# Performance work log

Measured on AMD Instinct MI355X. Metric: run time of the kernel, lower is better.

Reference implementation:

```python
import jax, jax.numpy as jnp
import numpy as np

B, S, D = 2, 2048, 2048
H, KVH = 16, 8
HD = D // H          # 128
REP = H // KVH       # 2
FF = 5504
EPS = 1e-5
THETA = 1e6


def rotate_half(x):
    h = x.shape[-1] // 2
    return jnp.concatenate([-x[..., h:], x[..., :h]], axis=-1)


def rms_norm(x, g):
    v = jnp.mean(x.astype(jnp.float32) ** 2, axis=-1, keepdims=True)
    return (x * jax.lax.rsqrt(v + EPS)).astype(x.dtype) * g


def setup_inputs() -> dict:
    key = jax.random.key(0)
    ks = jax.random.split(key, 10)
    # RoPE tables [S, HD]
    inv_freq = 1.0 / (THETA ** (np.arange(0, HD, 2, dtype=np.float32) / HD))
    t = np.arange(S, dtype=np.float32)
    freqs = np.outer(t, inv_freq)                      # [S, HD/2]
    emb = np.concatenate([freqs, freqs], axis=-1)      # [S, HD]
    sc = 0.02
    return {
        "x": jax.random.normal(ks[0], (B, S, D), jnp.float32),
        "cos": jnp.asarray(np.cos(emb)),
        "sin": jnp.asarray(np.sin(emb)),
        "wq": jax.random.normal(ks[1], (H * HD, D), jnp.float32) * sc,
        "wk": jax.random.normal(ks[2], (KVH * HD, D), jnp.float32) * sc,
        "wv": jax.random.normal(ks[3], (KVH * HD, D), jnp.float32) * sc,
        "wo": jax.random.normal(ks[4], (D, H * HD), jnp.float32) * sc,
        "w_gate": jax.random.normal(ks[5], (FF, D), jnp.float32) * sc,
        "w_up": jax.random.normal(ks[6], (FF, D), jnp.float32) * sc,
        "w_down": jax.random.normal(ks[7], (D, FF), jnp.float32) * sc,
        "g1": jnp.ones((D,), jnp.float32),
        "g2": jnp.ones((D,), jnp.float32),
    }


def reference(x, cos, sin, wq, wk, wv, wo, w_gate, w_up, w_down, g1, g2):
    # ---- attention sub-block ----
    h = rms_norm(x, g1)
    q = (h @ wq.T).reshape(B, S, H, HD)
    k = (h @ wk.T).reshape(B, S, KVH, HD)
    v = (h @ wv.T).reshape(B, S, KVH, HD)
    # RoPE: cos/sin [S,HD] -> broadcast over (B, S, heads, HD) via unsqueeze at head dim
    c = cos[:S][:, None, :]
    s = sin[:S][:, None, :]
    q = q * c + rotate_half(q) * s
    k = k * c + rotate_half(k) * s
    # GQA repeat_kv (repeat_interleave on head dim), then bshd -> bhsd
    k = jnp.repeat(k, REP, axis=2).transpose(0, 2, 1, 3)
    v = jnp.repeat(v, REP, axis=2).transpose(0, 2, 1, 3)
    q = q.transpose(0, 2, 1, 3)
    scores = jnp.einsum("bhqd,bhkd->bhqk", q, k) / jnp.sqrt(jnp.float32(HD))
    causal = jnp.triu(jnp.full((S, S), -jnp.inf, jnp.float32), k=1)
    scores = scores + causal[None, None]
    attn = jax.nn.softmax(scores.astype(jnp.float32), axis=-1).astype(scores.dtype)
    out = jnp.einsum("bhqk,bhkd->bhqd", attn, v)
    out = out.transpose(0, 2, 1, 3).reshape(B, S, H * HD)
    x = x + out @ wo.T
    # ---- SwiGLU MLP sub-block ----
    h2 = rms_norm(x, g2)
    mlp = (jax.nn.silu(h2 @ w_gate.T) * (h2 @ w_up.T)) @ w_down.T
    return x + mlp
```

## Files before the change

### kernel.cpp

```cpp
#include <hip/hip_runtime.h>


#define DM 2048
#define SEQ 2048
#define HD 128
#define FF_ 5504
#define QK_SCALE_L2E 0.12751744f

typedef __bf16 bf16x8 __attribute__((ext_vector_type(8)));
typedef float f32x4 __attribute__((ext_vector_type(4)));
typedef float f32x16 __attribute__((ext_vector_type(16)));
typedef unsigned short u16x8 __attribute__((ext_vector_type(8)));
typedef unsigned int u32x4 __attribute__((ext_vector_type(4)));

typedef __attribute__((address_space(1))) void* gas1;
typedef __attribute__((address_space(3))) void* las3;
#define GLDS16(g, s) __builtin_amdgcn_global_load_lds((gas1)(g), (las3)(s), 16, 0, 0)

static __device__ __forceinline__ float bf2f(unsigned short u) {
  union { unsigned int i; float f; } c; c.i = ((unsigned int)u) << 16; return c.f;
}
static __device__ __forceinline__ unsigned short f2bf(float f) {
  __bf16 b = (__bf16)f;
  return __builtin_bit_cast(unsigned short, b);
}
static __device__ __forceinline__ unsigned int pk2(float a, float b) {
  return (unsigned int)f2bf(a) | ((unsigned int)f2bf(b) << 16);
}
static __device__ __forceinline__ float fexp2(float x) { return exp2f(x); }

__global__ __launch_bounds__(256) void k_conv(const float* __restrict__ src,
                                              unsigned short* __restrict__ dst) {
  size_t i = (size_t)(blockIdx.x * 256 + threadIdx.x) * 8;
  float4 a = *(const float4*)&src[i];
  float4 b = *(const float4*)&src[i + 4];
  u16x8 o;
  o[0] = f2bf(a.x); o[1] = f2bf(a.y); o[2] = f2bf(a.z); o[3] = f2bf(a.w);
  o[4] = f2bf(b.x); o[5] = f2bf(b.y); o[6] = f2bf(b.z); o[7] = f2bf(b.w);
  *(u16x8*)&dst[i] = o;
}

__global__ __launch_bounds__(256) void k_conv_gu(const float* __restrict__ g,
                                                 const float* __restrict__ u,
                                                 unsigned short* __restrict__ dst) {
  int i = blockIdx.x * 256 + threadIdx.x;
  int row = i >> 8;
  int c8 = (i & 255) * 8;
  int t = row >> 8, r = row & 255;
  const float* src = (r < 128) ? (g + (size_t)(t * 128 + r) * DM + c8)
                               : (u + (size_t)(t * 128 + (r - 128)) * DM + c8);
  float4 a = *(const float4*)src;
  float4 b = *(const float4*)(src + 4);
  u16x8 o;
  o[0] = f2bf(a.x); o[1] = f2bf(a.y); o[2] = f2bf(a.z); o[3] = f2bf(a.w);
  o[4] = f2bf(b.x); o[5] = f2bf(b.y); o[6] = f2bf(b.z); o[7] = f2bf(b.w);
  *(u16x8*)&dst[(size_t)row * DM + c8] = o;
}

__global__ __launch_bounds__(256) void k_rmsnorm(const float* __restrict__ x,
                                                 const float* __restrict__ g,
                                                 unsigned short* __restrict__ out) {
  int row = blockIdx.x, tid = threadIdx.x;
  const float* xr = x + (size_t)row * DM;
  float4 a = *(const float4*)&xr[tid * 8];
  float4 b = *(const float4*)&xr[tid * 8 + 4];
  float ss = a.x * a.x + a.y * a.y + a.z * a.z + a.w * a.w +
             b.x * b.x + b.y * b.y + b.z * b.z + b.w * b.w;
#pragma unroll
  for (int off = 32; off > 0; off >>= 1) ss += __shfl_xor(ss, off, 64);
  __shared__ float red[4];
  if ((tid & 63) == 0) red[tid >> 6] = ss;
  __syncthreads();
  float rs = rsqrtf((red[0] + red[1] + red[2] + red[3]) * (1.0f / DM) + 1e-5f);
  float4 ga = *(const float4*)&g[tid * 8];
  float4 gb = *(const float4*)&g[tid * 8 + 4];
  u16x8 o;
  o[0] = f2bf(a.x * rs * ga.x); o[1] = f2bf(a.y * rs * ga.y);
  o[2] = f2bf(a.z * rs * ga.z); o[3] = f2bf(a.w * rs * ga.w);
  o[4] = f2bf(b.x * rs * gb.x); o[5] = f2bf(b.y * rs * gb.y);
  o[6] = f2bf(b.z * rs * gb.z); o[7] = f2bf(b.w * rs * gb.w);
  *(u16x8*)&out[(size_t)row * DM + tid * 8] = o;
}

__global__ __launch_bounds__(256) void k_rope(unsigned short* __restrict__ qkv,
                                              const float* __restrict__ cosT,
                                              const float* __restrict__ sinT) {
  int idx = blockIdx.x * 256 + threadIdx.x;
  int j = idx & 63;
  int hh = (idx >> 6) % 24;
  int tok = idx / (64 * 24);
  int s = tok & (SEQ - 1);
  int colbase = (hh < 16) ? hh * HD : DM + (hh - 16) * HD;
  unsigned short* p = qkv + (size_t)tok * 4096 + colbase;
  float lo = bf2f(p[j]), hi = bf2f(p[j + 64]);
  const float* cr = cosT + (size_t)s * HD;
  const float* sr = sinT + (size_t)s * HD;
  float nl = lo * cr[j] - hi * sr[j];
  float nh = hi * cr[j + 64] + lo * sr[j + 64];
  if (hh < 16) { nl *= QK_SCALE_L2E; nh *= QK_SCALE_L2E; }
  p[j] = f2bf(nl);
  p[j + 64] = f2bf(nh);
}

template <int BN, int EPI, int PIPE>
__global__ __launch_bounds__(512, 2) void k_gemm8(
    const unsigned short* __restrict__ A, const unsigned short* __restrict__ Bt,
    unsigned short* __restrict__ outB, float* __restrict__ outF,
    const float* __restrict__ res, int N, int K) {
  constexpr int NF = BN / 64;
  constexpr int BSTMT = BN / 128;
  constexpr int ABY = 256 * 64;
  constexpr int BBY = BN * 64;
  constexpr int BUF = ABY + BBY;
  constexpr int VPK = 2 + BSTMT;
  constexpr int NBUF = PIPE ? 2 : 4;
  __shared__ __attribute__((aligned(16))) unsigned char smem[NBUF * BUF];

  const int tid = threadIdx.x, w = tid >> 6, l = tid & 63;
  const int wr = w >> 2, wc = w & 3, lr = l & 15, lg = l >> 4;
  const int nwg = gridDim.x, bid = blockIdx.x;
  const int bswz = (bid & 7) * (nwg >> 3) + (bid >> 3);
  const int mt = bswz & 15, nt = bswz >> 4;
  const int m0 = mt * 256, n0 = nt * BN;
  const int nk = K >> 5;

  const int srow = w * 16 + (l >> 2);
  const int sg8 = ((l & 3) ^ ((l >> 3) & 3)) * 8;
  const unsigned short* Asrc = A + (size_t)(m0 + srow) * K + sg8;
  const unsigned short* Bsrc = Bt + (size_t)(n0 + srow) * K + sg8;
  const int aoff = (wr * 128 + lr) * 64 + ((lg ^ ((lr >> 1) & 3)) << 4);
  const int boff = (wc * (BN / 4) + lr) * 64 + ((lg ^ ((lr >> 1) & 3)) << 4);

  auto stageA = [&](int kt) {
    unsigned char* bb = smem + (kt & (NBUF - 1)) * BUF;
#pragma unroll
    for (int i = 0; i < 2; i++)
      GLDS16(Asrc + (size_t)i * 128 * K + kt * 32, bb + (i * 512 + w * 64) * 16);
  };
  auto stageB = [&](int kt) {
    unsigned char* bb = smem + (kt & (NBUF - 1)) * BUF + ABY;
#pragma unroll
    for (int i = 0; i < BSTMT; i++)
      GLDS16(Bsrc + (size_t)i * 128 * K + kt * 32, bb + (i * 512 + w * 64) * 16);
  };

  f32x4 acc[8][NF] = {};

  if constexpr (PIPE == 1) {
    stageA(0); stageB(0);
    asm volatile("s_waitcnt vmcnt(0)" ::: "memory");
    __builtin_amdgcn_s_barrier();
    for (int kt = 0; kt < nk; kt++) {
      unsigned char* ba = smem + (kt & 1) * BUF;
      unsigned char* bb = ba + ABY;
      if (kt + 1 < nk) { stageA(kt + 1); stageB(kt + 1); }
      bf16x8 am[8], bnf[NF];
#pragma unroll
      for (int m = 0; m < 8; m++) am[m] = *(const bf16x8*)(ba + aoff + m * 1024);
#pragma unroll
      for (int n = 0; n < NF; n++) bnf[n] = *(const bf16x8*)(bb + boff + n * 1024);
      __builtin_amdgcn_s_setprio(1);
#pragma unroll
      for (int m = 0; m < 8; m++)
#pragma unroll
        for (int n = 0; n < NF; n++)
          acc[m][n] = __builtin_amdgcn_mfma_f32_16x16x32_bf16(am[m], bnf[n], acc[m][n], 0, 0, 0);
      __builtin_amdgcn_s_setprio(0);
      asm volatile("s_waitcnt vmcnt(0)" ::: "memory");
      __builtin_amdgcn_s_barrier();
    }
  } else {
    for (int kt = 0; kt < 3; kt++) { stageA(kt); stageB(kt); }
    asm volatile("s_waitcnt vmcnt(%0)" ::"i"(2 * VPK) : "memory");
    __builtin_amdgcn_s_barrier();
    for (int kt = 0; kt < nk; kt++) {
      unsigned char* ba = smem + (kt & 3) * BUF;
      unsigned char* bb = ba + ABY;
      const bool st = (kt + 3) < nk;
      bf16x8 am[8], bnf[NF];
#pragma unroll
      for (int m = 0; m < 8; m++) am[m] = *(const bf16x8*)(ba + aoff + m * 1024);
#pragma unroll
      for (int n = 0; n < NF; n++) bnf[n] = *(const bf16x8*)(bb + boff + n * 1024);
      if (st) { stageA(kt + 3); stageB(kt + 3); }
      __builtin_amdgcn_s_barrier();
      __builtin_amdgcn_s_setprio(1);
#pragma unroll
      for (int m = 0; m < 8; m++)
#pragma unroll
        for (int n = 0; n < NF; n++)
          acc[m][n] = __builtin_amdgcn_mfma_f32_16x16x32_bf16(am[m], bnf[n], acc[m][n], 0, 0, 0);
      __builtin_amdgcn_s_setprio(0);
      if (kt <= nk - 4)      asm volatile("s_waitcnt vmcnt(%0)" ::"i"(2 * VPK) : "memory");
      else if (kt == nk - 3) asm volatile("s_waitcnt vmcnt(%0)" ::"i"(VPK) : "memory");
      else if (kt == nk - 2) asm volatile("s_waitcnt vmcnt(0)" ::: "memory");
      __builtin_amdgcn_s_barrier();
    }
  }

  const int rbase = wr * 128 + lg * 4;
  const int cbase = wc * (BN / 4) + lr;
  if constexpr (EPI == 0) {
#pragma unroll
    for (int m = 0; m < 8; m++)
#pragma unroll
      for (int n = 0; n < NF; n++)
#pragma unroll
        for (int j = 0; j < 4; j++)
          outB[(size_t)(m0 + rbase + m * 16 + j) * N + n0 + cbase + n * 16] =
              f2bf(acc[m][n][j]);
  } else if constexpr (EPI == 1) {
#pragma unroll
    for (int m = 0; m < 8; m++)
#pragma unroll
      for (int n = 0; n < NF; n++)
#pragma unroll
        for (int j = 0; j < 4; j++) {
          size_t o = (size_t)(m0 + rbase + m * 16 + j) * N + n0 + cbase + n * 16;
          outF[o] = res[o] + acc[m][n][j];
        }
  } else {
    float* gl = (float*)smem;
    const int ab = n0 >> 1;
    __syncthreads();
#pragma unroll
    for (int half = 0; half < 2; half++) {
      if (wr == half && wc < 2) {
#pragma unroll
        for (int m = 0; m < 8; m++)
#pragma unroll
          for (int n = 0; n < NF; n++)
#pragma unroll
            for (int j = 0; j < 4; j++)
              gl[(m * 16 + lg * 4 + j) * 128 + wc * 64 + n * 16 + lr] = acc[m][n][j];
      }
      __syncthreads();
      if (wr == half && wc >= 2) {
#pragma unroll
        for (int m = 0; m < 8; m++)
#pragma unroll
          for (int n = 0; n < NF; n++)
#pragma unroll
            for (int j = 0; j < 4; j++) {
              int rl = m * 16 + lg * 4 + j;
              int cl = (wc - 2) * 64 + n * 16 + lr;
              float g = gl[rl * 128 + cl];
              float s = g / (1.0f + __expf(-g));
              outB[(size_t)(m0 + half * 128 + rl) * FF_ + ab + cl] = f2bf(s * acc[m][n][j]);
            }
      }
      __syncthreads();
    }
  }
}

__global__ __launch_bounds__(256) void k_attn2(const unsigned short* __restrict__ qkv,
                                               unsigned short* __restrict__ out) {
  __shared__ __attribute__((aligned(16))) unsigned short lK[2][64 * 128];
  __shared__ __attribute__((aligned(16))) unsigned short lV[2][128 * 64];
  const float NEG = -3.0e38f;
  int bx = blockIdx.x;
  int qtile = 15 - (bx >> 5);
  int hb = bx & 31;
  int h = hb & 15, b = hb >> 4;
  int q0 = qtile * 128;
  int tid = threadIdx.x, w = tid >> 6, l = tid & 63;
  int l31 = l & 31, half2 = l >> 5;
  const unsigned short* base = qkv + (size_t)b * SEQ * 4096;
  const unsigned short* Kp = base + 2048 + (h >> 1) * HD;
  const unsigned short* Vp = base + 3072 + (h >> 1) * HD;
  const int qw = q0 + w * 32;

  bf16x8 qf[8];
  {
    const unsigned short* qrow = base + (size_t)(qw + l31) * 4096 + h * HD + half2 * 8;
#pragma unroll
    for (int d = 0; d < 8; d++) qf[d] = *(const bf16x8*)(qrow + d * 16);
  }

  f32x16 oacc[4] = {};
  float mrow = NEG, lsum = 0.0f;

  const int vp = tid & 31, vdc = tid >> 5;
  u16x8 va0, va1, vb0, vb1;

  auto stageK = [&](int t) {
    unsigned char* dst = (unsigned char*)lK[t & 1];
#pragma unroll
    for (int i = 0; i < 4; i++) {
      int c = i * 256 + tid;
      int row = c >> 4;
      int g = (c & 15) ^ (row & 7);
      GLDS16(Kp + (size_t)(t * 64 + row) * 4096 + g * 8, dst + (i * 256 + w * 64) * 16);
    }
  };
  auto loadV = [&](int t) {
    const unsigned short* vr = Vp + (size_t)(t * 64 + vp * 2) * 4096 + vdc * 16;
    va0 = *(const u16x8*)(vr);
    va1 = *(const u16x8*)(vr + 8);
    vb0 = *(const u16x8*)(vr + 4096);
    vb1 = *(const u16x8*)(vr + 4096 + 8);
  };

  const int nt = (q0 >> 6) + 2;
  stageK(0);
  loadV(0);

  for (int t = 0; t < nt; t++) {
    __syncthreads();
    {
      unsigned char* lv = (unsigned char*)lV[t & 1];
#pragma unroll
      for (int j = 0; j < 16; j++) {
        int dd = vdc * 16 + j;
        unsigned short lo = (j < 8) ? va0[j] : va1[j - 8];
        unsigned short hi = (j < 8) ? vb0[j] : vb1[j - 8];
        unsigned int pkv = (unsigned int)lo | ((unsigned int)hi << 16);
        *(unsigned int*)(lv + dd * 128 + (((vp >> 2) ^ (dd & 7)) * 16) + (vp & 3) * 4) = pkv;
      }
    }
    __syncthreads();
    if (t + 1 < nt) { stageK(t + 1); loadV(t + 1); }
    const int kv0 = t * 64;
    if (kv0 <= qw + 31) {
      f32x16 sc[2] = {};
      const unsigned char* lk = (const unsigned char*)lK[t & 1];
#pragma unroll
      for (int hh = 0; hh < 2; hh++) {
        int kk = hh * 32 + l31;
        const unsigned char* krow = lk + kk * 256;
#pragma unroll
        for (int d = 0; d < 8; d++) {
          bf16x8 kf = *(const bf16x8*)(krow + (((d * 2 + half2) ^ (kk & 7)) * 16));
          sc[hh] = __builtin_amdgcn_mfma_f32_32x32x16_bf16(kf, qf[d], sc[hh], 0, 0, 0);
        }
      }
      const int qa = qw + l31;
      if (kv0 + 63 > qw) {
#pragma unroll
        for (int hh = 0; hh < 2; hh++)
#pragma unroll
          for (int r = 0; r < 16; r++) {
            int kva = kv0 + hh * 32 + (r & 3) + 8 * (r >> 2) + 4 * half2;
            if (kva > qa) sc[hh][r] = NEG;
          }
      }
      float mx = sc[0][0];
#pragma unroll
      for (int r = 1; r < 16; r++) mx = fmaxf(mx, sc[0][r]);
#pragma unroll
      for (int r = 0; r < 16; r++) mx = fmaxf(mx, sc[1][r]);
      mx = fmaxf(mx, __shfl_xor(mx, 32));
      bool ok = (mx <= mrow + 11.0f);
      if (__ballot(ok) != ~0ull) {
        float mnew = fmaxf(mrow, mx);
        float fct = fexp2(mrow - mnew);
        mrow = mnew;
        lsum *= fct;
#pragma unroll
        for (int r = 0; r < 16; r++) {
          int rr = (r & 3) + 8 * (r >> 2) + 4 * half2;
          float fr = __shfl(fct, rr);
#pragma unroll
          for (int d = 0; d < 4; d++) oacc[d][r] *= fr;
        }
      }
      float ps = 0.0f;
#pragma unroll
      for (int hh = 0; hh < 2; hh++)
#pragma unroll
        for (int r = 0; r < 16; r++) {
          float e = fexp2(sc[hh][r] - mrow);
          sc[hh][r] = e;
          ps += e;
        }
      ps += __shfl_xor(ps, 32);
      lsum += ps;
      const unsigned char* lv = (const unsigned char*)lV[t & 1];
#pragma unroll
      for (int s = 0; s < 4; s++) {
        const int hh = s >> 1;
        const int r0 = (s & 1) * 8;
        unsigned int lo0, lo1, hi0, hi1;
        if (hh == 0) {
          lo0 = pk2(sc[0][r0 + 0], sc[0][r0 + 1]); lo1 = pk2(sc[0][r0 + 2], sc[0][r0 + 3]);
          hi0 = pk2(sc[0][r0 + 4], sc[0][r0 + 5]); hi1 = pk2(sc[0][r0 + 6], sc[0][r0 + 7]);
        } else {
          lo0 = pk2(sc[1][r0 + 0], sc[1][r0 + 1]); lo1 = pk2(sc[1][r0 + 2], sc[1][r0 + 3]);
          hi0 = pk2(sc[1][r0 + 4], sc[1][r0 + 5]); hi1 = pk2(sc[1][r0 + 6], sc[1][r0 + 7]);
        }
        unsigned int s0 = half2 ? lo0 : hi0, s1 = half2 ? lo1 : hi1;
        unsigned int rc0 = (unsigned int)__shfl_xor((int)s0, 32);
        unsigned int rc1 = (unsigned int)__shfl_xor((int)s1, 32);
        u32x4 fr;
        fr[0] = half2 ? rc0 : lo0; fr[1] = half2 ? rc1 : lo1;
        fr[2] = half2 ? hi0 : rc0; fr[3] = half2 ? hi1 : rc1;
        bf16x8 pa = __builtin_bit_cast(bf16x8, fr);
#pragma unroll
        for (int d = 0; d < 4; d++) {
          int dd = d * 32 + l31;
          bf16x8 vf = *(const bf16x8*)(lv + dd * 128 + (((s * 2 + half2) ^ (dd & 7)) * 16));
          oacc[d] = __builtin_amdgcn_mfma_f32_32x32x16_bf16(pa, vf, oacc[d], 0, 0, 0);
        }
      }
    }
  }
  float inv = 1.0f / lsum;
#pragma unroll
  for (int r = 0; r < 16; r++) {
    int rr = (r & 3) + 8 * (r >> 2) + 4 * half2;
    float ir = __shfl(inv, rr);
    size_t ob = ((size_t)(b * SEQ + qw + rr)) * 2048 + h * HD;
#pragma unroll
    for (int d = 0; d < 4; d++)
      out[ob + d * 32 + l31] = f2bf(oacc[d][r] * ir);
  }
}

extern "C" void kernel_launch(void* const* d_in, const int* in_sizes, int n_in,
                              void* d_out, int out_size, void* d_ws, size_t ws_size,
                              hipStream_t stream) {
  const float* x = (const float*)d_in[0];
  const float* cosT = (const float*)d_in[1];
  const float* sinT = (const float*)d_in[2];
  const float* wq = (const float*)d_in[3];
  const float* wk = (const float*)d_in[4];
  const float* wv = (const float*)d_in[5];
  const float* wo = (const float*)d_in[6];
  const float* wg = (const float*)d_in[7];
  const float* wu = (const float*)d_in[8];
  const float* wd = (const float*)d_in[9];
  const float* g1 = (const float*)d_in[10];
  const float* g2 = (const float*)d_in[11];
  float* out = (float*)d_out;
  char* ws = (char*)d_ws;

  unsigned short* wqkv = (unsigned short*)(ws + 0);
  unsigned short* hbuf = (unsigned short*)(ws + 16777216);
  unsigned short* qkv = (unsigned short*)(ws + 33554432);
  unsigned short* attn_o = (unsigned short*)(ws + 67108864);
  unsigned short* wo_bf = (unsigned short*)(ws + 83886080);
  unsigned short* wgu = (unsigned short*)(ws + 33554432);
  unsigned short* act = (unsigned short*)(ws + 92274688);
  unsigned short* wdown = (unsigned short*)(ws + 0);

  k_conv<<<2048, 256, 0, stream>>>(wq, wqkv);
  k_conv<<<1024, 256, 0, stream>>>(wk, wqkv + 4194304);
  k_conv<<<1024, 256, 0, stream>>>(wv, wqkv + 6291456);
  k_rmsnorm<<<4096, 256, 0, stream>>>(x, g1, hbuf);
  k_gemm8<128, 0, 1><<<512, 512, 0, stream>>>(hbuf, wqkv, qkv, nullptr, nullptr,
                                              4096, 2048);
  k_rope<<<24576, 256, 0, stream>>>(qkv, cosT, sinT);
  k_attn2<<<512, 256, 0, stream>>>(qkv, attn_o);
  k_conv<<<2048, 256, 0, stream>>>(wo, wo_bf);
  k_gemm8<128, 1, 0><<<256, 512, 0, stream>>>(attn_o, wo_bf, nullptr, out, x,
                                              2048, 2048);
  k_rmsnorm<<<4096, 256, 0, stream>>>(out, g2, hbuf);
  k_conv_gu<<<11008, 256, 0, stream>>>(wg, wu, wgu);
  k_gemm8<256, 2, 1><<<688, 512, 0, stream>>>(hbuf, wgu, act, nullptr, nullptr,
                                              11008, 2048);
  k_conv<<<5504, 256, 0, stream>>>(wd, wdown);
  k_gemm8<128, 1, 0><<<256, 512, 0, stream>>>(act, wdown, nullptr, out, out,
                                              2048, 5504);
}
```

Measured before the change: 623.3 us.

## Add 256x256x64 GEMM kernel with quarter-step interleaved prefetch for QKV and gate/up

Adds a new GEMM kernel that uses 256x256 output tiles with 64-wide K steps and double-buffered LDS. Each K step is split into four MFMA quarters, and the next tile's A and B halves are loaded between them so global-to-LDS traffic overlaps compute. The kernel uses an XOR-swizzled layout and fine-grained waitcnt/barrier placement. The QKV projection moves from 128-wide tiles to 256x256 tiles with half the blocks, and gate/up also uses the new kernel. The old two-stage PIPE path is removed. Larger tiles and one block per CU increase data reuse, but the risks are lower occupancy and fewer blocks to fill the device for QKV.

```diff
diff --git a/kernel.cpp b/kernel.cpp
--- a/kernel.cpp
+++ b/kernel.cpp
@@ -102,6 +102,180 @@
   p[j + 64] = f2bf(nh);
 }
 
+template <int EPI>
+__global__ __launch_bounds__(512, 1) void k_gemm8p(
+    const unsigned short* __restrict__ A, const unsigned short* __restrict__ Bt,
+    unsigned short* __restrict__ outB, float* __restrict__ outF,
+    const float* __restrict__ res, int N, int K) {
+  __shared__ __attribute__((aligned(16))) unsigned char smem[2][65536];
+  const int tid = threadIdx.x, w = tid >> 6, l = tid & 63;
+  const int wr = w >> 2, wc = w & 3, lr = l & 15, lg = l >> 4;
+  const int nwg = gridDim.x, bid = blockIdx.x;
+  const int bswz = (bid & 7) * (nwg >> 3) + (bid >> 3);
+  const int mt = bswz & 15, nt = bswz >> 4;
+  const int m0 = mt * 256, n0 = nt * 256;
+  const int nkt = K >> 6;
+
+  const int rA0 = tid >> 3;
+  const int rB0 = ((tid >> 8) << 6) + ((tid >> 3) & 31);
+  const int sc = ((tid & 7) ^ ((tid >> 3) & 7)) * 8;
+  const unsigned short* Abase = A + (size_t)(m0 + rA0) * K + sc;
+  const unsigned short* Bbase = Bt + (size_t)(n0 + rB0) * K + sc;
+
+  auto stA = [&](int kt, int h) {
+    unsigned char* dst = smem[kt & 1] + h * 16384;
+    const unsigned short* s = Abase + (size_t)(h * 64) * K + kt * 64;
+    GLDS16(s, dst + tid * 16);
+    GLDS16(s + (size_t)128 * K, dst + (512 + tid) * 16);
+  };
+  auto stB = [&](int kt, int h) {
+    unsigned char* dst = smem[kt & 1] + 32768 + h * 16384;
+    const unsigned short* s = Bbase + (size_t)(h * 32) * K + kt * 64;
+    GLDS16(s, dst + tid * 16);
+    GLDS16(s + (size_t)128 * K, dst + (512 + tid) * 16);
+  };
+
+  const int aRow = (wr * 64 + lr) * 128;
+  const int bRow = (wc * 32 + lr) * 128;
+  const int axr = lr & 7;
+#define RDA(BUF, M, KK)                                                        \
+  (*(const bf16x8*)((BUF) + ((M) >> 2) * 16384 + aRow + ((M) & 3) * 2048 +     \
+                    ((((KK) * 4 + lg) ^ axr) << 4)))
+#define RDB(BUF, NN, KK)                                                       \
+  (*(const bf16x8*)((BUF) + 32768 + ((NN) >> 1) * 16384 + bRow +               \
+                    ((NN) & 1) * 2048 + ((((KK) * 4 + lg) ^ axr) << 4)))
+
+  f32x4 acc[8][4] = {};
+  bf16x8 aq[4][2], bq0[2][2], bq1[2][2];
+
+  stA(0, 0); stB(0, 0); stB(0, 1); stA(0, 1);
+  asm volatile("s_waitcnt vmcnt(4)" ::: "memory");
+  __builtin_amdgcn_s_barrier();
+
+#define MMQ(MB, NB, BQ)                                                        \
+  _Pragma("unroll") for (int m = 0; m < 4; m++)                                \
+    _Pragma("unroll") for (int n = 0; n < 2; n++)                              \
+      _Pragma("unroll") for (int kk = 0; kk < 2; kk++)                         \
+          acc[(MB) + m][(NB) + n] = __builtin_amdgcn_mfma_f32_16x16x32_bf16(   \
+              aq[m][kk], BQ[n][kk], acc[(MB) + m][(NB) + n], 0, 0, 0);
+
+#define KT8(KT, ST, W1, W2, HASW4)                                             \
+  {                                                                            \
+    const unsigned char* buf = smem[(KT) & 1];                                 \
+                                                        \
+    _Pragma("unroll") for (int m = 0; m < 4; m++)                              \
+      _Pragma("unroll") for (int kk = 0; kk < 2; kk++)                         \
+          aq[m][kk] = RDA(buf, m, kk);                                         \
+    _Pragma("unroll") for (int n = 0; n < 2; n++)                              \
+      _Pragma("unroll") for (int kk = 0; kk < 2; kk++)                         \
+          bq0[n][kk] = RDB(buf, n, kk);                                        \
+    if (ST) stA((KT) + 1, 0);                                                  \
+    __builtin_amdgcn_s_barrier();                                              \
+    asm volatile("s_waitcnt lgkmcnt(0)" ::: "memory");                         \
+    __builtin_amdgcn_sched_barrier(0);                                         \
+    __builtin_amdgcn_s_setprio(1);                                             \
+    MMQ(0, 0, bq0)                                                             \
+    __builtin_amdgcn_s_setprio(0);                                             \
+    asm volatile("s_waitcnt vmcnt(%0)" ::"i"(W1) : "memory");                  \
+    __builtin_amdgcn_s_barrier();                                              \
+                                                        \
+    _Pragma("unroll") for (int n = 0; n < 2; n++)                              \
+      _Pragma("unroll") for (int kk = 0; kk < 2; kk++)                         \
+          bq1[n][kk] = RDB(buf, n + 2, kk);                                    \
+    if (ST) stB((KT) + 1, 0);                                                  \
+    __builtin_amdgcn_s_barrier();                                              \
+    asm volatile("s_waitcnt lgkmcnt(0)" ::: "memory");                         \
+    __builtin_amdgcn_sched_barrier(0);                                         \
+    __builtin_amdgcn_s_setprio(1);                                             \
+    MMQ(0, 2, bq1)                                                             \
+    __builtin_amdgcn_s_setprio(0);                                             \
+    asm volatile("s_waitcnt vmcnt(%0)" ::"i"(W2) : "memory");                  \
+    __builtin_amdgcn_s_barrier();                                              \
+                                                        \
+    _Pragma("unroll") for (int m = 0; m < 4; m++)                              \
+      _Pragma("unroll") for (int kk = 0; kk < 2; kk++)                         \
+          aq[m][kk] = RDA(buf, m + 4, kk);                                     \
+    if (ST) stB((KT) + 1, 1);                                                  \
+    __builtin_amdgcn_s_barrier();                                              \
+    asm volatile("s_waitcnt lgkmcnt(0)" ::: "memory");                         \
+    __builtin_amdgcn_sched_barrier(0);                                         \
+    __builtin_amdgcn_s_setprio(1);                                             \
+    MMQ(4, 2, bq1)                                                             \
+    __builtin_amdgcn_s_setprio(0);                                             \
+    __builtin_amdgcn_s_barrier();                                              \
+                                                        \
+    if (ST) stA((KT) + 1, 1);                                                  \
+    __builtin_amdgcn_s_barrier();                                              \
+    __builtin_amdgcn_s_setprio(1);                                             \
+    MMQ(4, 0, bq0)                                                             \
+    __builtin_amdgcn_s_setprio(0);                                             \
+    if (HASW4) asm volatile("s_waitcnt vmcnt(4)" ::: "memory");                \
+    __builtin_amdgcn_s_barrier();                                              \
+  }
+
+  for (int kt = 0; kt < nkt - 1; kt++) KT8(kt, true, 4, 4, true);
+  KT8(nkt - 1, false, 2, 0, false);
+#undef KT8
+#undef MMQ
+#undef RDA
+#undef RDB
+
+  const int rbase = wr * 128 + lg * 4;
+  const int cbase = wc * 64 + lr;
+  if constexpr (EPI == 0) {
+#pragma unroll
+    for (int m = 0; m < 8; m++)
+#pragma unroll
+      for (int n = 0; n < 4; n++)
+#pragma unroll
+        for (int j = 0; j < 4; j++)
+          outB[(size_t)(m0 + rbase + m * 16 + j) * N + n0 + cbase + n * 16] =
+              f2bf(acc[m][n][j]);
+  } else if constexpr (EPI == 1) {
+#pragma unroll
+    for (int m = 0; m < 8; m++)
+#pragma unroll
+      for (int n = 0; n < 4; n++)
+#pragma unroll
+        for (int j = 0; j < 4; j++) {
+          size_t o = (size_t)(m0 + rbase + m * 16 + j) * N + n0 + cbase + n * 16;
+          outF[o] = res[o] + acc[m][n][j];
+        }
+  } else {
+    float* gl = (float*)smem;
+    const int ab = n0 >> 1;
+    __syncthreads();
+#pragma unroll
+    for (int half = 0; half < 2; half++) {
+      if (wr == half && wc < 2) {
+#pragma unroll
+        for (int m = 0; m < 8; m++)
+#pragma unroll
+          for (int n = 0; n < 4; n++)
+#pragma unroll
+            for (int j = 0; j < 4; j++)
+              gl[(m * 16 + lg * 4 + j) * 128 + wc * 64 + n * 16 + lr] = acc[m][n][j];
+      }
+      __syncthreads();
+      if (wr == half && wc >= 2) {
+#pragma unroll
+        for (int m = 0; m < 8; m++)
+#pragma unroll
+          for (int n = 0; n < 4; n++)
+#pragma unroll
+            for (int j = 0; j < 4; j++) {
+              int rl = m * 16 + lg * 4 + j;
+              int cl = (wc - 2) * 64 + n * 16 + lr;
+              float g = gl[rl * 128 + cl];
+              float s = g / (1.0f + __expf(-g));
+              outB[(size_t)(m0 + half * 128 + rl) * FF_ + ab + cl] = f2bf(s * acc[m][n][j]);
+            }
+      }
+      __syncthreads();
+    }
+  }
+}
+
 template <int BN, int EPI, int PIPE>
 __global__ __launch_bounds__(512, 2) void k_gemm8(
     const unsigned short* __restrict__ A, const unsigned short* __restrict__ Bt,
@@ -113,8 +287,7 @@
   constexpr int BBY = BN * 64;
   constexpr int BUF = ABY + BBY;
   constexpr int VPK = 2 + BSTMT;
-  constexpr int NBUF = PIPE ? 2 : 4;
-  __shared__ __attribute__((aligned(16))) unsigned char smem[NBUF * BUF];
+  __shared__ __attribute__((aligned(16))) unsigned char smem[4 * BUF];
 
   const int tid = threadIdx.x, w = tid >> 6, l = tid & 63;
   const int wr = w >> 2, wc = w & 3, lr = l & 15, lg = l >> 4;
@@ -132,13 +305,13 @@
   const int boff = (wc * (BN / 4) + lr) * 64 + ((lg ^ ((lr >> 1) & 3)) << 4);
 
   auto stageA = [&](int kt) {
-    unsigned char* bb = smem + (kt & (NBUF - 1)) * BUF;
+    unsigned char* bb = smem + (kt & 3) * BUF;
 #pragma unroll
     for (int i = 0; i < 2; i++)
       GLDS16(Asrc + (size_t)i * 128 * K + kt * 32, bb + (i * 512 + w * 64) * 16);
   };
   auto stageB = [&](int kt) {
-    unsigned char* bb = smem + (kt & (NBUF - 1)) * BUF + ABY;
+    unsigned char* bb = smem + (kt & 3) * BUF + ABY;
 #pragma unroll
     for (int i = 0; i < BSTMT; i++)
       GLDS16(Bsrc + (size_t)i * 128 * K + kt * 32, bb + (i * 512 + w * 64) * 16);
@@ -146,56 +319,31 @@
 
   f32x4 acc[8][NF] = {};
 
-  if constexpr (PIPE == 1) {
-    stageA(0); stageB(0);
-    asm volatile("s_waitcnt vmcnt(0)" ::: "memory");
+  for (int kt = 0; kt < 3; kt++) { stageA(kt); stageB(kt); }
+  asm volatile("s_waitcnt vmcnt(%0)" ::"i"(2 * VPK) : "memory");
+  __builtin_amdgcn_s_barrier();
+  for (int kt = 0; kt < nk; kt++) {
+    unsigned char* ba = smem + (kt & 3) * BUF;
+    unsigned char* bb = ba + ABY;
+    const bool st = (kt + 3) < nk;
+    bf16x8 am[8], bnf[NF];
+#pragma unroll
+    for (int m = 0; m < 8; m++) am[m] = *(const bf16x8*)(ba + aoff + m * 1024);
+#pragma unroll
+    for (int n = 0; n < NF; n++) bnf[n] = *(const bf16x8*)(bb + boff + n * 1024);
+    if (st) { stageA(kt + 3); stageB(kt + 3); }
     __builtin_amdgcn_s_barrier();
-    for (int kt = 0; kt < nk; kt++) {
-      unsigned char* ba = smem + (kt & 1) * BUF;
-      unsigned char* bb = ba + ABY;
-      if (kt + 1 < nk) { stageA(kt + 1); stageB(kt + 1); }
-      bf16x8 am[8], bnf[NF];
-#pragma unroll
-      for (int m = 0; m < 8; m++) am[m] = *(const bf16x8*)(ba + aoff + m * 1024);
-#pragma unroll
-      for (int n = 0; n < NF; n++) bnf[n] = *(const bf16x8*)(bb + boff + n * 1024);
-      __builtin_amdgcn_s_setprio(1);
-#pragma unroll
-      for (int m = 0; m < 8; m++)
-#pragma unroll
-        for (int n = 0; n < NF; n++)
-          acc[m][n] = __builtin_amdgcn_mfma_f32_16x16x32_bf16(am[m], bnf[n], acc[m][n], 0, 0, 0);
-      __builtin_amdgcn_s_setprio(0);
-      asm volatile("s_waitcnt vmcnt(0)" ::: "memory");
-      __builtin_amdgcn_s_barrier();
-    }
-  } else {
-    for (int kt = 0; kt < 3; kt++) { stageA(kt); stageB(kt); }
-    asm volatile("s_waitcnt vmcnt(%0)" ::"i"(2 * VPK) : "memory");
+    __builtin_amdgcn_s_setprio(1);
+#pragma unroll
+    for (int m = 0; m < 8; m++)
+#pragma unroll
+      for (int n = 0; n < NF; n++)
+        acc[m][n] = __builtin_amdgcn_mfma_f32_16x16x32_bf16(am[m], bnf[n], acc[m][n], 0, 0, 0);
+    __builtin_amdgcn_s_setprio(0);
+    if (kt <= nk - 4)      asm volatile("s_waitcnt vmcnt(%0)" ::"i"(2 * VPK) : "memory");
+    else if (kt == nk - 3) asm volatile("s_waitcnt vmcnt(%0)" ::"i"(VPK) : "memory");
+    else if (kt == nk - 2) asm volatile("s_waitcnt vmcnt(0)" ::: "memory");
     __builtin_amdgcn_s_barrier();
-    for (int kt = 0; kt < nk; kt++) {
-      unsigned char* ba = smem + (kt & 3) * BUF;
-      unsigned char* bb = ba + ABY;
-      const bool st = (kt + 3) < nk;
-      bf16x8 am[8], bnf[NF];
-#pragma unroll
-      for (int m = 0; m < 8; m++) am[m] = *(const bf16x8*)(ba + aoff + m * 1024);
-#pragma unroll
-      for (int n = 0; n < NF; n++) bnf[n] = *(const bf16x8*)(bb + boff + n * 1024);
-      if (st) { stageA(kt + 3); stageB(kt + 3); }
-      __builtin_amdgcn_s_barrier();
-      __builtin_amdgcn_s_setprio(1);
-#pragma unroll
-      for (int m = 0; m < 8; m++)
-#pragma unroll
-        for (int n = 0; n < NF; n++)
-          acc[m][n] = __builtin_amdgcn_mfma_f32_16x16x32_bf16(am[m], bnf[n], acc[m][n], 0, 0, 0);
-      __builtin_amdgcn_s_setprio(0);
-      if (kt <= nk - 4)      asm volatile("s_waitcnt vmcnt(%0)" ::"i"(2 * VPK) : "memory");
-      else if (kt == nk - 3) asm volatile("s_waitcnt vmcnt(%0)" ::"i"(VPK) : "memory");
-      else if (kt == nk - 2) asm volatile("s_waitcnt vmcnt(0)" ::: "memory");
-      __builtin_amdgcn_s_barrier();
-    }
   }
 
   const int rbase = wr * 128 + lg * 4;
@@ -209,7 +357,7 @@
         for (int j = 0; j < 4; j++)
           outB[(size_t)(m0 + rbase + m * 16 + j) * N + n0 + cbase + n * 16] =
               f2bf(acc[m][n][j]);
-  } else if constexpr (EPI == 1) {
+  } else {
 #pragma unroll
     for (int m = 0; m < 8; m++)
 #pragma unroll
@@ -219,38 +367,6 @@
           size_t o = (size_t)(m0 + rbase + m * 16 + j) * N + n0 + cbase + n * 16;
           outF[o] = res[o] + acc[m][n][j];
         }
-  } else {
-    float* gl = (float*)smem;
-    const int ab = n0 >> 1;
-    __syncthreads();
-#pragma unroll
-    for (int half = 0; half < 2; half++) {
-      if (wr == half && wc < 2) {
-#pragma unroll
-        for (int m = 0; m < 8; m++)
-#pragma unroll
-          for (int n = 0; n < NF; n++)
-#pragma unroll
-            for (int j = 0; j < 4; j++)
-              gl[(m * 16 + lg * 4 + j) * 128 + wc * 64 + n * 16 + lr] = acc[m][n][j];
-      }
-      __syncthreads();
-      if (wr == half && wc >= 2) {
-#pragma unroll
-        for (int m = 0; m < 8; m++)
-#pragma unroll
-          for (int n = 0; n < NF; n++)
-#pragma unroll
-            for (int j = 0; j < 4; j++) {
-              int rl = m * 16 + lg * 4 + j;
-              int cl = (wc - 2) * 64 + n * 16 + lr;
-              float g = gl[rl * 128 + cl];
-              float s = g / (1.0f + __expf(-g));
-              outB[(size_t)(m0 + half * 128 + rl) * FF_ + ab + cl] = f2bf(s * acc[m][n][j]);
-            }
-      }
-      __syncthreads();
-    }
   }
 }
 
@@ -448,8 +564,8 @@
   k_conv<<<1024, 256, 0, stream>>>(wk, wqkv + 4194304);
   k_conv<<<1024, 256, 0, stream>>>(wv, wqkv + 6291456);
   k_rmsnorm<<<4096, 256, 0, stream>>>(x, g1, hbuf);
-  k_gemm8<128, 0, 1><<<512, 512, 0, stream>>>(hbuf, wqkv, qkv, nullptr, nullptr,
-                                              4096, 2048);
+  k_gemm8p<0><<<256, 512, 0, stream>>>(hbuf, wqkv, qkv, nullptr, nullptr,
+                                       4096, 2048);
   k_rope<<<24576, 256, 0, stream>>>(qkv, cosT, sinT);
   k_attn2<<<512, 256, 0, stream>>>(qkv, attn_o);
   k_conv<<<2048, 256, 0, stream>>>(wo, wo_bf);
@@ -457,8 +573,8 @@
                                               2048, 2048);
   k_rmsnorm<<<4096, 256, 0, stream>>>(out, g2, hbuf);
   k_conv_gu<<<11008, 256, 0, stream>>>(wg, wu, wgu);
-  k_gemm8<256, 2, 1><<<688, 512, 0, stream>>>(hbuf, wgu, act, nullptr, nullptr,
-                                              11008, 2048);
+  k_gemm8p<2><<<688, 512, 0, stream>>>(hbuf, wgu, act, nullptr, nullptr,
+                                       11008, 2048);
   k_conv<<<5504, 256, 0, stream>>>(wd, wdown);
   k_gemm8<128, 1, 0><<<256, 512, 0, stream>>>(act, wdown, nullptr, out, out,
                                               2048, 5504);
```

New measurement: 595.7 us. 4.4% less time.
